# Kernel tuning notes

Hardware: AMD Instinct MI355X
Metric: run time of the kernel (lower is better)

The kernel has to match this reference:

```python
import jax, jax.numpy as jnp
import numpy as np

B, L, W = 4096, 30, 5          # batch, MAX_TOKEN_LENGTH, WINDOW_SIZE
A, E = 30, 128                 # ALPHABET_SIZE, embedding dim
C = 40                         # OUT_CHANNELS
H, T = 128, 3                  # LSTM_UNITS, num CRF tags
LIN = W * C                    # 200
EPS = 1e-5


def setup_inputs():
    key = jax.random.key(0)
    ks = jax.random.split(key, 24)
    def rn(k, shape, s=0.1):
        return jax.random.normal(k, shape, jnp.float32) * s
    return {
        'x': jax.random.randint(ks[0], (B, L, W), 0, A, jnp.int32),
        'emb': rn(ks[1], (A, E), 1.0),
        'conv_w': rn(ks[2], (C, E, 3)),
        'conv_b': rn(ks[3], (C,)),
        'bn1_g': 1.0 + rn(ks[4], (C,)),
        'bn1_b': rn(ks[5], (C,)),
        'bn1_m': rn(ks[6], (C,)),
        'bn1_v': 0.5 + jax.random.uniform(ks[7], (C,), jnp.float32),
        'w_ih_f': rn(ks[8], (4 * H, LIN)),
        'w_hh_f': rn(ks[9], (4 * H, H)),
        'b_f': rn(ks[10], (4 * H,)),
        'w_ih_b': rn(ks[11], (4 * H, LIN)),
        'w_hh_b': rn(ks[12], (4 * H, H)),
        'b_b': rn(ks[13], (4 * H,)),
        'bn2_g': 1.0 + rn(ks[14], (2 * H,)),
        'bn2_b': rn(ks[15], (2 * H,)),
        'bn2_m': rn(ks[16], (2 * H,)),
        'bn2_v': 0.5 + jax.random.uniform(ks[17], (2 * H,), jnp.float32),
        'fc_w': rn(ks[18], (T, 2 * H)),
        'fc_b': rn(ks[19], (T,)),
        'trans': rn(ks[20], (T, T)),
        'start_t': rn(ks[21], (T,)),
        'end_t': rn(ks[22], (T,)),
    }


def _lstm_dir(seq, w_ih, w_hh, b, reverse):
    # seq: [B, L, F]; torch gate order i, f, g, o
    xs = jnp.einsum('blf,gf->lbg', seq, w_ih) + b  # [L, B, 4H]
    h0 = jnp.zeros((seq.shape[0], H), seq.dtype)
    def step(carry, xt):
        h, c = carry
        z = xt + h @ w_hh.T
        i, f, g, o = jnp.split(z, 4, axis=-1)
        c = jax.nn.sigmoid(f) * c + jax.nn.sigmoid(i) * jnp.tanh(g)
        h = jax.nn.sigmoid(o) * jnp.tanh(c)
        return (h, c), h
    _, hs = jax.lax.scan(step, (h0, h0), xs, reverse=reverse)
    return hs.transpose(1, 0, 2)  # [B, L, H]


def _viterbi(emis, mask, trans, start_t, end_t):
    # emis: [B, L, T], mask: [B, L] bool
    score = start_t + emis[:, 0]                      # [B, T]
    def step(score, inp):
        e_t, m_t = inp                                # [B, T], [B]
        cand = score[:, :, None] + trans              # [B, Tprev, Tnext]
        ptr = jnp.argmax(cand, axis=1)                # [B, T]
        new = jnp.max(cand, axis=1) + e_t
        return jnp.where(m_t[:, None], new, score), ptr
    score, hist = jax.lax.scan(
        step, score, (emis[:, 1:].transpose(1, 0, 2), mask[:, 1:].T))
    score = score + end_t
    best = jnp.max(score, axis=1)                     # [B] path scores
    last = jnp.argmax(score, axis=1)                  # [B]
    def back(tag, inp):
        h_t, m_t = inp
        prev = jnp.take_along_axis(h_t, tag[:, None], axis=1)[:, 0]
        tag = jnp.where(m_t, prev, tag)
        return tag, tag
    _, ys = jax.lax.scan(back, last, (hist, mask[:, 1:].T), reverse=True)
    tags = jnp.concatenate([ys, last[None]], axis=0).T  # [B, L]
    return best, tags


def reference(x, emb, conv_w, conv_b, bn1_g, bn1_b, bn1_m, bn1_v,
              w_ih_f, w_hh_f, b_f, w_ih_b, w_hh_b, b_b,
              bn2_g, bn2_b, bn2_m, bn2_v, fc_w, fc_b, trans, start_t, end_t):
    mask = x[:, :, 2] > 0                             # [B, L]
    e = emb[x.reshape(B * L, W)]                      # [N, W, E]  (dropout=eval noop)
    e = e.transpose(0, 2, 1)                          # [N, E, W]
    y = jax.lax.conv_general_dilated(
        e, conv_w, (1,), [(1, 1)],
        dimension_numbers=('NCH', 'OIH', 'NCH')) + conv_b[:, None]
    # BatchNorm1d (inference, running stats)
    y = (y - bn1_m[:, None]) * (bn1_g / jnp.sqrt(bn1_v + EPS))[:, None] + bn1_b[:, None]
    y = jax.nn.relu(y)
    # MaxPool1d(k=3, stride=1, pad=1): length preserved
    y = jax.lax.reduce_window(y, -jnp.inf, jax.lax.max,
                              (1, 1, 3), (1, 1, 1),
                              [(0, 0), (0, 0), (1, 1)])
    y = y.reshape(B, L, LIN)                          # torch.flatten is channel-major = row-major reshape
    hf = _lstm_dir(y, w_ih_f, w_hh_f, b_f, False)
    hb = _lstm_dir(y, w_ih_b, w_hh_b, b_b, True)
    h = jnp.concatenate([hf, hb], axis=-1)            # [B, L, 2H]
    h = (h - bn2_m) * (bn2_g / jnp.sqrt(bn2_v + EPS)) + bn2_b
    emis = h @ fc_w.T + fc_b                          # [B, L, T]
    return _viterbi(emis, mask, trans, start_t, end_t)
```

## Files before the change

### kernel.cpp

```cpp
#include <hip/hip_runtime.h>
#include <math.h>

#define BB    4096
#define LL    30
#define WW    5
#define CC    40
#define HH    128
#define TT    3
#define KA    328
#define NB    32
#define FSTR  232
#define HSTR  136
#define CW    1056

#define WS_P    0
#define WS_BC   3600
#define WS_BG   3648
#define WS_WFC  4672
#define WS_EB   5440
#define WS_WBF  5504
#define WS_EMIS (5504 + 540672)

typedef __bf16 bf16x8 __attribute__((ext_vector_type(8)));
typedef float  f32x4  __attribute__((ext_vector_type(4)));
typedef unsigned short u16x8 __attribute__((ext_vector_type(8)));

__device__ __forceinline__ float sigm(float x) {
    return __builtin_amdgcn_rcpf(1.0f + __expf(-x));
}
__device__ __forceinline__ float tanh_fast(float x) {
    return 2.0f * __builtin_amdgcn_rcpf(1.0f + __expf(-2.0f * x)) - 1.0f;
}
__device__ __forceinline__ unsigned short f2bf(float f) {
    unsigned u = __builtin_bit_cast(unsigned, f);
    return (unsigned short)((u + 0x7FFFu + ((u >> 16) & 1u)) >> 16);
}
__device__ __forceinline__ float bf2f(unsigned short h) {
    unsigned u = ((unsigned)h) << 16;
    return __builtin_bit_cast(float, u);
}

__global__ void prep_kernel(const float* __restrict__ emb, const float* __restrict__ conv_w,
                            const float* __restrict__ conv_b,
                            const float* __restrict__ bn1_g, const float* __restrict__ bn1_b,
                            const float* __restrict__ bn1_m, const float* __restrict__ bn1_v,
                            const float* __restrict__ w_ih_f, const float* __restrict__ w_hh_f,
                            const float* __restrict__ b_f,
                            const float* __restrict__ w_ih_b, const float* __restrict__ w_hh_b,
                            const float* __restrict__ b_b,
                            const float* __restrict__ bn2_g, const float* __restrict__ bn2_b,
                            const float* __restrict__ bn2_m, const float* __restrict__ bn2_v,
                            const float* __restrict__ fc_w, const float* __restrict__ fc_b,
                            float* __restrict__ ws)
{
    const int gid = blockIdx.x * blockDim.x + threadIdx.x;
    const int gsz = gridDim.x * blockDim.x;

    for (int idx = gid; idx < 3600; idx += gsz) {
        int k = idx / 1200, rem = idx % 1200, a = rem / 40, c = rem % 40;
        float s1 = bn1_g[c] / sqrtf(bn1_v[c] + 1e-5f);
        float acc = 0.f;
        for (int e = 0; e < 128; ++e)
            acc += emb[a * 128 + e] * conv_w[(c * 128 + e) * 3 + k];
        ws[WS_P + idx] = acc * s1;
    }
    for (int c = gid; c < CC; c += gsz) {
        float s1 = bn1_g[c] / sqrtf(bn1_v[c] + 1e-5f);
        ws[WS_BC + c] = (conv_b[c] - bn1_m[c]) * s1 + bn1_b[c];
    }
    for (int i = gid; i < 1024; i += gsz) {
        int d = i >> 9, g = i & 511;
        ws[WS_BG + i] = d ? b_b[g] : b_f[g];
    }
    for (int i = gid; i < 768; i += gsz) {
        int d = i / 384, r = i % 384, t = r / 128, u = r % 128;
        int j = d * 128 + u;
        float s2 = bn2_g[j] / sqrtf(bn2_v[j] + 1e-5f);
        ws[WS_WFC + i] = fc_w[t * 256 + j] * s2;
    }
    for (int t = gid; t < TT; t += gsz) {
        float acc = fc_b[t];
        for (int j = 0; j < 256; ++j) {
            float s2 = bn2_g[j] / sqrtf(bn2_v[j] + 1e-5f);
            acc += fc_w[t * 256 + j] * (bn2_b[j] - bn2_m[j] * s2);
        }
        ws[WS_EB + t] = acc;
    }
    unsigned short* wsu = (unsigned short*)ws;
    for (int i = gid; i < 2 * 512 * CW; i += gsz) {
        int d = i / (512 * CW), r = i % (512 * CW);
        int n = r / CW, q = r % CW;
        int Ks = q / 96, t = q % 96, s = t / 32, k32 = t % 32;
        int k = Ks * 32 + k32;
        int u = n >> 2, g = n & 3, row = g * 128 + u;
        const float* wih = d ? w_ih_b : w_ih_f;
        const float* whh = d ? w_hh_b : w_hh_f;
        float w = (k < 200) ? wih[row * 200 + k]
                            : ((k >= 224) ? whh[row * 128 + (k - 224)] : 0.f);
        unsigned short t0 = f2bf(w);
        float r1 = w - bf2f(t0);
        unsigned short t1 = f2bf(r1);
        unsigned short t2 = f2bf(r1 - bf2f(t1));
        wsu[2 * WS_WBF + i] = (s == 0) ? t0 : ((s == 1) ? t1 : t2);
    }
}

__global__ __launch_bounds__(512, 1)
void lstm_kernel(const int* __restrict__ x, float* __restrict__ ws)
{
    __shared__ unsigned short Fh[2][NB * FSTR], Fl[2][NB * FSTR], Fm[2][NB * FSTR];
    __shared__ unsigned short Hh[NB * HSTR], Hl[NB * HSTR], Hm[NB * HSTR];
    __shared__ float Pp_s[3600];
    __shared__ float Wfc_s[384];
    __shared__ float biasC_s[40];

    const int tid = threadIdx.x;
    const int d   = blockIdx.x & 1;
    const int b0  = (blockIdx.x >> 1) * NB;

    const unsigned short* __restrict__ Wb =
        (const unsigned short*)ws + 2 * WS_WBF + d * (512 * CW);
    float* emis = ws + WS_EMIS + d * (BB * LL * TT);

    for (int i = tid; i < 3600; i += 512) Pp_s[i] = ws[WS_P + i];
    for (int i = tid; i < 384;  i += 512) Wfc_s[i] = ws[WS_WFC + d * 384 + i];
    for (int i = tid; i < 40;   i += 512) biasC_s[i] = ws[WS_BC + i];
    for (int i = tid; i < NB * FSTR; i += 512) {
        ((unsigned*)Fh)[i] = 0u; ((unsigned*)Fl)[i] = 0u; ((unsigned*)Fm)[i] = 0u;
    }
    for (int i = tid; i < NB * HSTR / 2; i += 512) {
        ((unsigned*)Hh)[i] = 0u; ((unsigned*)Hl)[i] = 0u; ((unsigned*)Hm)[i] = 0u;
    }

    const int lane = tid & 63;
    const int wv   = tid >> 6;
    const int quad = lane >> 4;
    const int ml   = lane & 15;

    const unsigned short* __restrict__ Wn[4] = {
        Wb + (wv * 64 +  0 + ml) * CW + quad * 8,
        Wb + (wv * 64 + 16 + ml) * CW + quad * 8,
        Wb + (wv * 64 + 32 + ml) * CW + quad * 8,
        Wb + (wv * 64 + 48 + ml) * CW + quad * 8
    };

    const float* bgp = ws + WS_BG + d * 512;
    int   un[4];
    float bIv[4], bFv[4], bGv[4], bOv[4];
    #pragma unroll
    for (int nt = 0; nt < 4; ++nt) {
        int u = wv * 16 + nt * 4 + quad;
        un[nt]  = u;
        bIv[nt] = bgp[u];
        bFv[nt] = bgp[128 + u];
        bGv[nt] = bgp[256 + u];
        bOv[nt] = bgp[384 + u];
    }

    float cst[2][4];
    #pragma unroll
    for (int mt = 0; mt < 2; ++mt)
        #pragma unroll
        for (int nt = 0; nt < 4; ++nt) cst[mt][nt] = 0.f;

    __syncthreads();

#define DO_FEATURES(LPOS, BUF)                                                 \
    for (int p = tid; p < NB * CC; p += 512) {                                 \
        int bb = p / CC, c = p % CC;                                           \
        const int* tok = x + (((b0 + bb) * LL) + (LPOS)) * WW;                 \
        int t0 = tok[0], t1 = tok[1], t2 = tok[2], t3 = tok[3], t4 = tok[4];   \
        float bc = biasC_s[c];                                                 \
        float a0 = bc + Pp_s[(30 + t0) * 40 + c] + Pp_s[(60 + t1) * 40 + c];   \
        float a1 = bc + Pp_s[t0 * 40 + c] + Pp_s[(30 + t1) * 40 + c] + Pp_s[(60 + t2) * 40 + c]; \
        float a2 = bc + Pp_s[t1 * 40 + c] + Pp_s[(30 + t2) * 40 + c] + Pp_s[(60 + t3) * 40 + c]; \
        float a3 = bc + Pp_s[t2 * 40 + c] + Pp_s[(30 + t3) * 40 + c] + Pp_s[(60 + t4) * 40 + c]; \
        float a4 = bc + Pp_s[t3 * 40 + c] + Pp_s[(30 + t4) * 40 + c];          \
        a0 = fmaxf(a0, 0.f); a1 = fmaxf(a1, 0.f); a2 = fmaxf(a2, 0.f);         \
        a3 = fmaxf(a3, 0.f); a4 = fmaxf(a4, 0.f);                              \
        float f[5];                                                            \
        f[0] = fmaxf(a0, a1);                                                  \
        f[1] = fmaxf(fmaxf(a0, a1), a2);                                       \
        f[2] = fmaxf(fmaxf(a1, a2), a3);                                       \
        f[3] = fmaxf(fmaxf(a2, a3), a4);                                       \
        f[4] = fmaxf(a3, a4);                                                  \
        int base = bb * FSTR + c * 5;                                          \
        _Pragma("unroll")                                                      \
        for (int j = 0; j < 5; ++j) {                                          \
            unsigned short h0 = f2bf(f[j]);                                    \
            float r1 = f[j] - bf2f(h0);                                        \
            unsigned short h1 = f2bf(r1);                                      \
            unsigned short h2 = f2bf(r1 - bf2f(h1));                           \
            Fh[BUF][base + j] = h0;                                            \
            Fl[BUF][base + j] = h1;                                            \
            Fm[BUF][base + j] = h2;                                            \
        }                                                                      \
    }

    {
        const int l0 = d ? (LL - 1) : 0;
        DO_FEATURES(l0, 0)
    }
    __syncthreads();

    for (int step = 0; step < LL; ++step) {
        const int fb = step & 1;

        f32x4 acc[2][4];
        #pragma unroll
        for (int mt = 0; mt < 2; ++mt)
            #pragma unroll
            for (int nt = 0; nt < 4; ++nt)
                acc[mt][nt] = (f32x4){0.f, 0.f, 0.f, 0.f};

#define WLOAD(B, P, KS)                                                        \
        {                                                                      \
            B[0] = *(const bf16x8*)((P) + (KS) * 96);                          \
            B[1] = *(const bf16x8*)((P) + (KS) * 96 + 32);                     \
            B[2] = *(const bf16x8*)((P) + (KS) * 96 + 64);                     \
        }
#define GEMM6(B, NT)                                                           \
        {                                                                      \
            acc[0][NT] = __builtin_amdgcn_mfma_f32_16x16x32_bf16(B[0], a0[0], acc[0][NT], 0, 0, 0); \
            acc[0][NT] = __builtin_amdgcn_mfma_f32_16x16x32_bf16(B[0], a0[1], acc[0][NT], 0, 0, 0); \
            acc[0][NT] = __builtin_amdgcn_mfma_f32_16x16x32_bf16(B[1], a0[0], acc[0][NT], 0, 0, 0); \
            acc[0][NT] = __builtin_amdgcn_mfma_f32_16x16x32_bf16(B[1], a0[1], acc[0][NT], 0, 0, 0); \
            acc[0][NT] = __builtin_amdgcn_mfma_f32_16x16x32_bf16(B[2], a0[0], acc[0][NT], 0, 0, 0); \
            acc[0][NT] = __builtin_amdgcn_mfma_f32_16x16x32_bf16(B[0], a0[2], acc[0][NT], 0, 0, 0); \
            acc[1][NT] = __builtin_amdgcn_mfma_f32_16x16x32_bf16(B[0], a1[0], acc[1][NT], 0, 0, 0); \
            acc[1][NT] = __builtin_amdgcn_mfma_f32_16x16x32_bf16(B[0], a1[1], acc[1][NT], 0, 0, 0); \
            acc[1][NT] = __builtin_amdgcn_mfma_f32_16x16x32_bf16(B[1], a1[0], acc[1][NT], 0, 0, 0); \
            acc[1][NT] = __builtin_amdgcn_mfma_f32_16x16x32_bf16(B[1], a1[1], acc[1][NT], 0, 0, 0); \
            acc[1][NT] = __builtin_amdgcn_mfma_f32_16x16x32_bf16(B[2], a1[0], acc[1][NT], 0, 0, 0); \
            acc[1][NT] = __builtin_amdgcn_mfma_f32_16x16x32_bf16(B[0], a1[2], acc[1][NT], 0, 0, 0); \
        }

        {
            bf16x8 wbuf[2][4][3];
            #pragma unroll
            for (int nt = 0; nt < 4; ++nt)
                WLOAD(wbuf[0][nt], Wn[nt], 0)

            #pragma unroll
            for (int Ks = 0; Ks < 11; ++Ks) {
                const int cur = Ks & 1, nxt = cur ^ 1;
                if (Ks < 10) {
                    #pragma unroll
                    for (int nt = 0; nt < 4; ++nt)
                        WLOAD(wbuf[nxt][nt], Wn[nt], Ks + 1)
                }
                bf16x8 a0[3], a1[3];
                if (Ks < 7) {
                    const int ko = Ks * 32 + quad * 8;
                    a0[0] = *(const bf16x8*)&Fh[fb][ml * FSTR + ko];
                    a0[1] = *(const bf16x8*)&Fl[fb][ml * FSTR + ko];
                    a0[2] = *(const bf16x8*)&Fm[fb][ml * FSTR + ko];
                    a1[0] = *(const bf16x8*)&Fh[fb][(16 + ml) * FSTR + ko];
                    a1[1] = *(const bf16x8*)&Fl[fb][(16 + ml) * FSTR + ko];
                    a1[2] = *(const bf16x8*)&Fm[fb][(16 + ml) * FSTR + ko];
                } else {
                    const int ko = (Ks - 7) * 32 + quad * 8;
                    a0[0] = *(const bf16x8*)&Hh[ml * HSTR + ko];
                    a0[1] = *(const bf16x8*)&Hl[ml * HSTR + ko];
                    a0[2] = *(const bf16x8*)&Hm[ml * HSTR + ko];
                    a1[0] = *(const bf16x8*)&Hh[(16 + ml) * HSTR + ko];
                    a1[1] = *(const bf16x8*)&Hl[(16 + ml) * HSTR + ko];
                    a1[2] = *(const bf16x8*)&Hm[(16 + ml) * HSTR + ko];
                }
                GEMM6(wbuf[cur][0], 0)
                GEMM6(wbuf[cur][1], 1)
                GEMM6(wbuf[cur][2], 2)
                GEMM6(wbuf[cur][3], 3)
            }
        }
#undef WLOAD
#undef GEMM6

        if (step + 1 < LL) {
            const int lnext = d ? (LL - 2 - step) : (step + 1);
            DO_FEATURES(lnext, (step + 1) & 1)
        }
        if (step > 0 && tid < 192) {
            const int lprev = d ? (LL - step) : (step - 1);
            int bb = tid / 6, r6 = tid % 6, t = r6 >> 1, seg = r6 & 1;
            int hb = bb * HSTR + seg * 64;
            const float* wfc = &Wfc_s[t * 128 + seg * 64];
            float s = 0.f;
            #pragma unroll
            for (int i = 0; i < 8; ++i) {
                u16x8 v0 = *(const u16x8*)&Hh[hb + i * 8];
                u16x8 v1 = *(const u16x8*)&Hl[hb + i * 8];
                u16x8 v2 = *(const u16x8*)&Hm[hb + i * 8];
                #pragma unroll
                for (int j = 0; j < 8; ++j) {
                    float h = bf2f(v0[j]) + bf2f(v1[j]) + bf2f(v2[j]);
                    s += h * wfc[i * 8 + j];
                }
            }
            s += __shfl_xor(s, 1);
            if (seg == 0)
                emis[(((b0 + bb) * LL) + lprev) * TT + t] = s;
        }

        __syncthreads();

        #pragma unroll
        for (int mt = 0; mt < 2; ++mt) {
            #pragma unroll
            for (int nt = 0; nt < 4; ++nt) {
                float zi = acc[mt][nt][0] + bIv[nt];
                float zf = acc[mt][nt][1] + bFv[nt];
                float zg = acc[mt][nt][2] + bGv[nt];
                float zo = acc[mt][nt][3] + bOv[nt];
                float cn = sigm(zf) * cst[mt][nt] + sigm(zi) * tanh_fast(zg);
                cst[mt][nt] = cn;
                float h = sigm(zo) * tanh_fast(cn);
                unsigned short h0 = f2bf(h);
                float r1 = h - bf2f(h0);
                unsigned short h1 = f2bf(r1);
                unsigned short h2 = f2bf(r1 - bf2f(h1));
                int idx = (mt * 16 + ml) * HSTR + un[nt];
                Hh[idx] = h0;
                Hl[idx] = h1;
                Hm[idx] = h2;
            }
        }
        __syncthreads();
    }

    if (tid < 192) {
        const int llast = d ? 0 : (LL - 1);
        int bb = tid / 6, r6 = tid % 6, t = r6 >> 1, seg = r6 & 1;
        int hb = bb * HSTR + seg * 64;
        const float* wfc = &Wfc_s[t * 128 + seg * 64];
        float s = 0.f;
        #pragma unroll
        for (int i = 0; i < 8; ++i) {
            u16x8 v0 = *(const u16x8*)&Hh[hb + i * 8];
            u16x8 v1 = *(const u16x8*)&Hl[hb + i * 8];
            u16x8 v2 = *(const u16x8*)&Hm[hb + i * 8];
            #pragma unroll
            for (int j = 0; j < 8; ++j) {
                float h = bf2f(v0[j]) + bf2f(v1[j]) + bf2f(v2[j]);
                s += h * wfc[i * 8 + j];
            }
        }
        s += __shfl_xor(s, 1);
        if (seg == 0)
            emis[(((b0 + bb) * LL) + llast) * TT + t] = s;
    }
#undef DO_FEATURES
}

__global__ void viterbi_kernel(const int* __restrict__ x, const float* __restrict__ ws,
                               const float* __restrict__ trans,
                               const float* __restrict__ start_t,
                               const float* __restrict__ end_t,
                               float* __restrict__ out)
{
    int b = blockIdx.x * blockDim.x + threadIdx.x;
    if (b >= BB) return;
    const float* eF = ws + WS_EMIS;
    const float* eB = ws + WS_EMIS + BB * LL * TT;
    const float eb0 = ws[WS_EB + 0], eb1 = ws[WS_EB + 1], eb2 = ws[WS_EB + 2];
    float tr[9];
    #pragma unroll
    for (int i = 0; i < 9; ++i) tr[i] = trans[i];

    int base = b * LL * TT;
    float s0 = start_t[0] + eF[base + 0] + eB[base + 0] + eb0;
    float s1 = start_t[1] + eF[base + 1] + eB[base + 1] + eb1;
    float s2 = start_t[2] + eF[base + 2] + eB[base + 2] + eb2;

    unsigned hist[LL - 1];
    unsigned maskbits = 0;

    #pragma unroll
    for (int l = 1; l < LL; ++l) {
        bool m = x[(b * LL + l) * WW + 2] > 0;
        if (m) maskbits |= (1u << l);
        int idx = base + l * TT;
        float e0 = eF[idx + 0] + eB[idx + 0] + eb0;
        float e1 = eF[idx + 1] + eB[idx + 1] + eb1;
        float e2 = eF[idx + 2] + eB[idx + 2] + eb2;

        float ns[3]; int pt[3];
        #pragma unroll
        for (int nt = 0; nt < 3; ++nt) {
            float c0 = s0 + tr[0 * 3 + nt];
            float c1 = s1 + tr[1 * 3 + nt];
            float c2 = s2 + tr[2 * 3 + nt];
            int p = 0; float bc = c0;
            if (c1 > bc) { bc = c1; p = 1; }
            if (c2 > bc) { bc = c2; p = 2; }
            ns[nt] = bc; pt[nt] = p;
        }
        ns[0] += e0; ns[1] += e1; ns[2] += e2;
        hist[l - 1] = (unsigned)pt[0] | ((unsigned)pt[1] << 2) | ((unsigned)pt[2] << 4);
        if (m) { s0 = ns[0]; s1 = ns[1]; s2 = ns[2]; }
    }
    s0 += end_t[0]; s1 += end_t[1]; s2 += end_t[2];
    float best = s0; int last = 0;
    if (s1 > best) { best = s1; last = 1; }
    if (s2 > best) { best = s2; last = 2; }

    out[b] = best;
    float* tags = out + BB + b * LL;
    int tag = last;
    tags[LL - 1] = (float)last;
    #pragma unroll
    for (int l = LL - 1; l >= 1; --l) {
        int prev = (int)((hist[l - 1] >> (2 * tag)) & 3u);
        if (maskbits & (1u << l)) tag = prev;
        tags[l - 1] = (float)tag;
    }
}

extern "C" void kernel_launch(void* const* d_in, const int* in_sizes, int n_in,
                              void* d_out, int out_size, void* d_ws, size_t ws_size,
                              hipStream_t stream)
{
    const int*   x      = (const int*)  d_in[0];
    const float* emb    = (const float*)d_in[1];
    const float* conv_w = (const float*)d_in[2];
    const float* conv_b = (const float*)d_in[3];
    const float* bn1_g  = (const float*)d_in[4];
    const float* bn1_b  = (const float*)d_in[5];
    const float* bn1_m  = (const float*)d_in[6];
    const float* bn1_v  = (const float*)d_in[7];
    const float* w_ih_f = (const float*)d_in[8];
    const float* w_hh_f = (const float*)d_in[9];
    const float* b_f    = (const float*)d_in[10];
    const float* w_ih_b = (const float*)d_in[11];
    const float* w_hh_b = (const float*)d_in[12];
    const float* b_b    = (const float*)d_in[13];
    const float* bn2_g  = (const float*)d_in[14];
    const float* bn2_b  = (const float*)d_in[15];
    const float* bn2_m  = (const float*)d_in[16];
    const float* bn2_v  = (const float*)d_in[17];
    const float* fc_w   = (const float*)d_in[18];
    const float* fc_b   = (const float*)d_in[19];
    const float* trans  = (const float*)d_in[20];
    const float* start_t= (const float*)d_in[21];
    const float* end_t  = (const float*)d_in[22];

    float* ws  = (float*)d_ws;
    float* out = (float*)d_out;

    prep_kernel<<<256, 256, 0, stream>>>(emb, conv_w, conv_b,
                                         bn1_g, bn1_b, bn1_m, bn1_v,
                                         w_ih_f, w_hh_f, b_f,
                                         w_ih_b, w_hh_b, b_b,
                                         bn2_g, bn2_b, bn2_m, bn2_v,
                                         fc_w, fc_b, ws);
    lstm_kernel<<<256, 512, 0, stream>>>(x, ws);
    viterbi_kernel<<<16, 256, 0, stream>>>(x, ws, trans, start_t, end_t, out);
}
```

Before: 811.9 us.

## Specialize waves: split GEMM and feature/emission work across separate warps

Doubles the LSTM block to 1024 threads. Eight waves run the recurrent MFMA GEMM and the gate update. The other eight compute the next timestep's conv features and the previous step's emission projection at the same time. This aims to hide the serial feature and emission work behind the matrix multiply in each timestep. It risks register pressure from the larger launch bound, since the GEMM waves hold large weight and accumulator buffers.

```diff
diff --git a/kernel.cpp b/kernel.cpp
--- a/kernel.cpp
+++ b/kernel.cpp
@@ -9,6 +9,7 @@
 #define TT    3
 #define KA    328
 #define NB    32
+#define NT_   1024
 #define FSTR  232
 #define HSTR  136
 #define CW    1056
@@ -105,7 +106,7 @@
     }
 }
 
-__global__ __launch_bounds__(512, 1)
+__global__ __launch_bounds__(1024, 1)
 void lstm_kernel(const int* __restrict__ x, float* __restrict__ ws)
 {
     __shared__ unsigned short Fh[2][NB * FSTR], Fl[2][NB * FSTR], Fm[2][NB * FSTR];
@@ -122,51 +123,53 @@
         (const unsigned short*)ws + 2 * WS_WBF + d * (512 * CW);
     float* emis = ws + WS_EMIS + d * (BB * LL * TT);
 
-    for (int i = tid; i < 3600; i += 512) Pp_s[i] = ws[WS_P + i];
-    for (int i = tid; i < 384;  i += 512) Wfc_s[i] = ws[WS_WFC + d * 384 + i];
-    for (int i = tid; i < 40;   i += 512) biasC_s[i] = ws[WS_BC + i];
-    for (int i = tid; i < NB * FSTR; i += 512) {
+    for (int i = tid; i < 3600; i += NT_) Pp_s[i] = ws[WS_P + i];
+    for (int i = tid; i < 384;  i += NT_) Wfc_s[i] = ws[WS_WFC + d * 384 + i];
+    for (int i = tid; i < 40;   i += NT_) biasC_s[i] = ws[WS_BC + i];
+    for (int i = tid; i < NB * FSTR; i += NT_) {
         ((unsigned*)Fh)[i] = 0u; ((unsigned*)Fl)[i] = 0u; ((unsigned*)Fm)[i] = 0u;
     }
-    for (int i = tid; i < NB * HSTR / 2; i += 512) {
+    for (int i = tid; i < NB * HSTR / 2; i += NT_) {
         ((unsigned*)Hh)[i] = 0u; ((unsigned*)Hl)[i] = 0u; ((unsigned*)Hm)[i] = 0u;
     }
 
     const int lane = tid & 63;
     const int wv   = tid >> 6;
+    const bool is_gemm = (wv < 8);
     const int quad = lane >> 4;
     const int ml   = lane & 15;
 
+    const int gw = wv & 7;
     const unsigned short* __restrict__ Wn[4] = {
-        Wb + (wv * 64 +  0 + ml) * CW + quad * 8,
-        Wb + (wv * 64 + 16 + ml) * CW + quad * 8,
-        Wb + (wv * 64 + 32 + ml) * CW + quad * 8,
-        Wb + (wv * 64 + 48 + ml) * CW + quad * 8
+        Wb + (gw * 64 +  0 + ml) * CW + quad * 8,
+        Wb + (gw * 64 + 16 + ml) * CW + quad * 8,
+        Wb + (gw * 64 + 32 + ml) * CW + quad * 8,
+        Wb + (gw * 64 + 48 + ml) * CW + quad * 8
     };
-
     const float* bgp = ws + WS_BG + d * 512;
     int   un[4];
     float bIv[4], bFv[4], bGv[4], bOv[4];
     #pragma unroll
     for (int nt = 0; nt < 4; ++nt) {
-        int u = wv * 16 + nt * 4 + quad;
+        int u = gw * 16 + nt * 4 + quad;
         un[nt]  = u;
         bIv[nt] = bgp[u];
         bFv[nt] = bgp[128 + u];
         bGv[nt] = bgp[256 + u];
         bOv[nt] = bgp[384 + u];
     }
-
     float cst[2][4];
     #pragma unroll
     for (int mt = 0; mt < 2; ++mt)
         #pragma unroll
         for (int nt = 0; nt < 4; ++nt) cst[mt][nt] = 0.f;
 
+    const int atid = tid - 512;
+
     __syncthreads();
 
 #define DO_FEATURES(LPOS, BUF)                                                 \
-    for (int p = tid; p < NB * CC; p += 512) {                                 \
+    for (int p = atid; p < NB * CC; p += 512) {                                \
         int bb = p / CC, c = p % CC;                                           \
         const int* tok = x + (((b0 + bb) * LL) + (LPOS)) * WW;                 \
         int t0 = tok[0], t1 = tok[1], t2 = tok[2], t3 = tok[3], t4 = tok[4];   \
@@ -197,140 +200,144 @@
         }                                                                      \
     }
 
-    {
+    if (!is_gemm) {
         const int l0 = d ? (LL - 1) : 0;
         DO_FEATURES(l0, 0)
     }
     __syncthreads();
 
+    f32x4 acc[2][4];
+
     for (int step = 0; step < LL; ++step) {
         const int fb = step & 1;
 
-        f32x4 acc[2][4];
-        #pragma unroll
-        for (int mt = 0; mt < 2; ++mt)
+        if (is_gemm) {
             #pragma unroll
-            for (int nt = 0; nt < 4; ++nt)
-                acc[mt][nt] = (f32x4){0.f, 0.f, 0.f, 0.f};
+            for (int mt = 0; mt < 2; ++mt)
+                #pragma unroll
+                for (int nt = 0; nt < 4; ++nt)
+                    acc[mt][nt] = (f32x4){0.f, 0.f, 0.f, 0.f};
 
 #define WLOAD(B, P, KS)                                                        \
-        {                                                                      \
-            B[0] = *(const bf16x8*)((P) + (KS) * 96);                          \
-            B[1] = *(const bf16x8*)((P) + (KS) * 96 + 32);                     \
-            B[2] = *(const bf16x8*)((P) + (KS) * 96 + 64);                     \
-        }
+            {                                                                  \
+                B[0] = *(const bf16x8*)((P) + (KS) * 96);                      \
+                B[1] = *(const bf16x8*)((P) + (KS) * 96 + 32);                 \
+                B[2] = *(const bf16x8*)((P) + (KS) * 96 + 64);                 \
+            }
 #define GEMM6(B, NT)                                                           \
-        {                                                                      \
-            acc[0][NT] = __builtin_amdgcn_mfma_f32_16x16x32_bf16(B[0], a0[0], acc[0][NT], 0, 0, 0); \
-            acc[0][NT] = __builtin_amdgcn_mfma_f32_16x16x32_bf16(B[0], a0[1], acc[0][NT], 0, 0, 0); \
-            acc[0][NT] = __builtin_amdgcn_mfma_f32_16x16x32_bf16(B[1], a0[0], acc[0][NT], 0, 0, 0); \
-            acc[0][NT] = __builtin_amdgcn_mfma_f32_16x16x32_bf16(B[1], a0[1], acc[0][NT], 0, 0, 0); \
-            acc[0][NT] = __builtin_amdgcn_mfma_f32_16x16x32_bf16(B[2], a0[0], acc[0][NT], 0, 0, 0); \
-            acc[0][NT] = __builtin_amdgcn_mfma_f32_16x16x32_bf16(B[0], a0[2], acc[0][NT], 0, 0, 0); \
-            acc[1][NT] = __builtin_amdgcn_mfma_f32_16x16x32_bf16(B[0], a1[0], acc[1][NT], 0, 0, 0); \
-            acc[1][NT] = __builtin_amdgcn_mfma_f32_16x16x32_bf16(B[0], a1[1], acc[1][NT], 0, 0, 0); \
-            acc[1][NT] = __builtin_amdgcn_mfma_f32_16x16x32_bf16(B[1], a1[0], acc[1][NT], 0, 0, 0); \
-            acc[1][NT] = __builtin_amdgcn_mfma_f32_16x16x32_bf16(B[1], a1[1], acc[1][NT], 0, 0, 0); \
-            acc[1][NT] = __builtin_amdgcn_mfma_f32_16x16x32_bf16(B[2], a1[0], acc[1][NT], 0, 0, 0); \
-            acc[1][NT] = __builtin_amdgcn_mfma_f32_16x16x32_bf16(B[0], a1[2], acc[1][NT], 0, 0, 0); \
-        }
-
-        {
-            bf16x8 wbuf[2][4][3];
-            #pragma unroll
-            for (int nt = 0; nt < 4; ++nt)
-                WLOAD(wbuf[0][nt], Wn[nt], 0)
-
-            #pragma unroll
-            for (int Ks = 0; Ks < 11; ++Ks) {
-                const int cur = Ks & 1, nxt = cur ^ 1;
-                if (Ks < 10) {
-                    #pragma unroll
-                    for (int nt = 0; nt < 4; ++nt)
-                        WLOAD(wbuf[nxt][nt], Wn[nt], Ks + 1)
+            {                                                                  \
+                acc[0][NT] = __builtin_amdgcn_mfma_f32_16x16x32_bf16(B[0], a0[0], acc[0][NT], 0, 0, 0); \
+                acc[0][NT] = __builtin_amdgcn_mfma_f32_16x16x32_bf16(B[0], a0[1], acc[0][NT], 0, 0, 0); \
+                acc[0][NT] = __builtin_amdgcn_mfma_f32_16x16x32_bf16(B[1], a0[0], acc[0][NT], 0, 0, 0); \
+                acc[0][NT] = __builtin_amdgcn_mfma_f32_16x16x32_bf16(B[1], a0[1], acc[0][NT], 0, 0, 0); \
+                acc[0][NT] = __builtin_amdgcn_mfma_f32_16x16x32_bf16(B[2], a0[0], acc[0][NT], 0, 0, 0); \
+                acc[0][NT] = __builtin_amdgcn_mfma_f32_16x16x32_bf16(B[0], a0[2], acc[0][NT], 0, 0, 0); \
+                acc[1][NT] = __builtin_amdgcn_mfma_f32_16x16x32_bf16(B[0], a1[0], acc[1][NT], 0, 0, 0); \
+                acc[1][NT] = __builtin_amdgcn_mfma_f32_16x16x32_bf16(B[0], a1[1], acc[1][NT], 0, 0, 0); \
+                acc[1][NT] = __builtin_amdgcn_mfma_f32_16x16x32_bf16(B[1], a1[0], acc[1][NT], 0, 0, 0); \
+                acc[1][NT] = __builtin_amdgcn_mfma_f32_16x16x32_bf16(B[1], a1[1], acc[1][NT], 0, 0, 0); \
+                acc[1][NT] = __builtin_amdgcn_mfma_f32_16x16x32_bf16(B[2], a1[0], acc[1][NT], 0, 0, 0); \
+                acc[1][NT] = __builtin_amdgcn_mfma_f32_16x16x32_bf16(B[0], a1[2], acc[1][NT], 0, 0, 0); \
+            }
+            {
+                bf16x8 wbuf[2][4][3];
+                #pragma unroll
+                for (int nt = 0; nt < 4; ++nt)
+                    WLOAD(wbuf[0][nt], Wn[nt], 0)
+
+                #pragma unroll
+                for (int Ks = 0; Ks < 11; ++Ks) {
+                    const int cur = Ks & 1, nxt = cur ^ 1;
+                    if (Ks < 10) {
+                        #pragma unroll
+                        for (int nt = 0; nt < 4; ++nt)
+                            WLOAD(wbuf[nxt][nt], Wn[nt], Ks + 1)
+                    }
+                    bf16x8 a0[3], a1[3];
+                    if (Ks < 7) {
+                        const int ko = Ks * 32 + quad * 8;
+                        a0[0] = *(const bf16x8*)&Fh[fb][ml * FSTR + ko];
+                        a0[1] = *(const bf16x8*)&Fl[fb][ml * FSTR + ko];
+                        a0[2] = *(const bf16x8*)&Fm[fb][ml * FSTR + ko];
+                        a1[0] = *(const bf16x8*)&Fh[fb][(16 + ml) * FSTR + ko];
+                        a1[1] = *(const bf16x8*)&Fl[fb][(16 + ml) * FSTR + ko];
+                        a1[2] = *(const bf16x8*)&Fm[fb][(16 + ml) * FSTR + ko];
+                    } else {
+                        const int ko = (Ks - 7) * 32 + quad * 8;
+                        a0[0] = *(const bf16x8*)&Hh[ml * HSTR + ko];
+                        a0[1] = *(const bf16x8*)&Hl[ml * HSTR + ko];
+                        a0[2] = *(const bf16x8*)&Hm[ml * HSTR + ko];
+                        a1[0] = *(const bf16x8*)&Hh[(16 + ml) * HSTR + ko];
+                        a1[1] = *(const bf16x8*)&Hl[(16 + ml) * HSTR + ko];
+                        a1[2] = *(const bf16x8*)&Hm[(16 + ml) * HSTR + ko];
+                    }
+                    GEMM6(wbuf[cur][0], 0)
+                    GEMM6(wbuf[cur][1], 1)
+                    GEMM6(wbuf[cur][2], 2)
+                    GEMM6(wbuf[cur][3], 3)
                 }
-                bf16x8 a0[3], a1[3];
-                if (Ks < 7) {
-                    const int ko = Ks * 32 + quad * 8;
-                    a0[0] = *(const bf16x8*)&Fh[fb][ml * FSTR + ko];
-                    a0[1] = *(const bf16x8*)&Fl[fb][ml * FSTR + ko];
-                    a0[2] = *(const bf16x8*)&Fm[fb][ml * FSTR + ko];
-                    a1[0] = *(const bf16x8*)&Fh[fb][(16 + ml) * FSTR + ko];
-                    a1[1] = *(const bf16x8*)&Fl[fb][(16 + ml) * FSTR + ko];
-                    a1[2] = *(const bf16x8*)&Fm[fb][(16 + ml) * FSTR + ko];
-                } else {
-                    const int ko = (Ks - 7) * 32 + quad * 8;
-                    a0[0] = *(const bf16x8*)&Hh[ml * HSTR + ko];
-                    a0[1] = *(const bf16x8*)&Hl[ml * HSTR + ko];
-                    a0[2] = *(const bf16x8*)&Hm[ml * HSTR + ko];
-                    a1[0] = *(const bf16x8*)&Hh[(16 + ml) * HSTR + ko];
-                    a1[1] = *(const bf16x8*)&Hl[(16 + ml) * HSTR + ko];
-                    a1[2] = *(const bf16x8*)&Hm[(16 + ml) * HSTR + ko];
-                }
-                GEMM6(wbuf[cur][0], 0)
-                GEMM6(wbuf[cur][1], 1)
-                GEMM6(wbuf[cur][2], 2)
-                GEMM6(wbuf[cur][3], 3)
-            }
-        }
+            }
 #undef WLOAD
 #undef GEMM6
-
-        if (step + 1 < LL) {
-            const int lnext = d ? (LL - 2 - step) : (step + 1);
-            DO_FEATURES(lnext, (step + 1) & 1)
+        } else {
+            if (step + 1 < LL) {
+                const int lnext = d ? (LL - 2 - step) : (step + 1);
+                DO_FEATURES(lnext, (step + 1) & 1)
+            }
+            if (step > 0 && atid < 192) {
+                const int lprev = d ? (LL - step) : (step - 1);
+                int bb = atid / 6, r6 = atid % 6, t = r6 >> 1, seg = r6 & 1;
+                int hb = bb * HSTR + seg * 64;
+                const float* wfc = &Wfc_s[t * 128 + seg * 64];
+                float s = 0.f;
+                #pragma unroll
+                for (int i = 0; i < 8; ++i) {
+                    u16x8 v0 = *(const u16x8*)&Hh[hb + i * 8];
+                    u16x8 v1 = *(const u16x8*)&Hl[hb + i * 8];
+                    u16x8 v2 = *(const u16x8*)&Hm[hb + i * 8];
+                    #pragma unroll
+                    for (int j = 0; j < 8; ++j) {
+                        float h = bf2f(v0[j]) + bf2f(v1[j]) + bf2f(v2[j]);
+                        s += h * wfc[i * 8 + j];
+                    }
+                }
+                s += __shfl_xor(s, 1);
+                if (seg == 0)
+                    emis[(((b0 + bb) * LL) + lprev) * TT + t] = s;
+            }
         }
-        if (step > 0 && tid < 192) {
-            const int lprev = d ? (LL - step) : (step - 1);
-            int bb = tid / 6, r6 = tid % 6, t = r6 >> 1, seg = r6 & 1;
-            int hb = bb * HSTR + seg * 64;
-            const float* wfc = &Wfc_s[t * 128 + seg * 64];
-            float s = 0.f;
+
+        __syncthreads();
+
+        if (is_gemm) {
             #pragma unroll
-            for (int i = 0; i < 8; ++i) {
-                u16x8 v0 = *(const u16x8*)&Hh[hb + i * 8];
-                u16x8 v1 = *(const u16x8*)&Hl[hb + i * 8];
-                u16x8 v2 = *(const u16x8*)&Hm[hb + i * 8];
+            for (int mt = 0; mt < 2; ++mt) {
                 #pragma unroll
-                for (int j = 0; j < 8; ++j) {
-                    float h = bf2f(v0[j]) + bf2f(v1[j]) + bf2f(v2[j]);
-                    s += h * wfc[i * 8 + j];
+                for (int nt = 0; nt < 4; ++nt) {
+                    float zi = acc[mt][nt][0] + bIv[nt];
+                    float zf = acc[mt][nt][1] + bFv[nt];
+                    float zg = acc[mt][nt][2] + bGv[nt];
+                    float zo = acc[mt][nt][3] + bOv[nt];
+                    float cn = sigm(zf) * cst[mt][nt] + sigm(zi) * tanh_fast(zg);
+                    cst[mt][nt] = cn;
+                    float h = sigm(zo) * tanh_fast(cn);
+                    unsigned short h0 = f2bf(h);
+                    float r1 = h - bf2f(h0);
+                    unsigned short h1 = f2bf(r1);
+                    unsigned short h2 = f2bf(r1 - bf2f(h1));
+                    int idx = (mt * 16 + ml) * HSTR + un[nt];
+                    Hh[idx] = h0;
+                    Hl[idx] = h1;
+                    Hm[idx] = h2;
                 }
-            }
-            s += __shfl_xor(s, 1);
-            if (seg == 0)
-                emis[(((b0 + bb) * LL) + lprev) * TT + t] = s;
-        }
-
-        __syncthreads();
-
-        #pragma unroll
-        for (int mt = 0; mt < 2; ++mt) {
-            #pragma unroll
-            for (int nt = 0; nt < 4; ++nt) {
-                float zi = acc[mt][nt][0] + bIv[nt];
-                float zf = acc[mt][nt][1] + bFv[nt];
-                float zg = acc[mt][nt][2] + bGv[nt];
-                float zo = acc[mt][nt][3] + bOv[nt];
-                float cn = sigm(zf) * cst[mt][nt] + sigm(zi) * tanh_fast(zg);
-                cst[mt][nt] = cn;
-                float h = sigm(zo) * tanh_fast(cn);
-                unsigned short h0 = f2bf(h);
-                float r1 = h - bf2f(h0);
-                unsigned short h1 = f2bf(r1);
-                unsigned short h2 = f2bf(r1 - bf2f(h1));
-                int idx = (mt * 16 + ml) * HSTR + un[nt];
-                Hh[idx] = h0;
-                Hl[idx] = h1;
-                Hm[idx] = h2;
             }
         }
         __syncthreads();
     }
 
-    if (tid < 192) {
+    if (!is_gemm && atid < 192) {
         const int llast = d ? 0 : (LL - 1);
-        int bb = tid / 6, r6 = tid % 6, t = r6 >> 1, seg = r6 & 1;
+        int bb = atid / 6, r6 = atid % 6, t = r6 >> 1, seg = r6 & 1;
         int hb = bb * HSTR + seg * 64;
         const float* wfc = &Wfc_s[t * 128 + seg * 64];
         float s = 0.f;
@@ -453,6 +460,6 @@
                                          w_ih_b, w_hh_b, b_b,
                                          bn2_g, bn2_b, bn2_m, bn2_v,
                                          fc_w, fc_b, ws);
-    lstm_kernel<<<256, 512, 0, stream>>>(x, ws);
+    lstm_kernel<<<256, 1024, 0, stream>>>(x, ws);
     viterbi_kernel<<<16, 256, 0, stream>>>(x, ws, trans, start_t, end_t, out);
 }
```

Result: no change. 816.9 us (+0.6%).
